# Optimization experiments

Measured on AMD Instinct MI355X. Metric: run time of the kernel, lower is better.

The kernel has to match this reference:

```python
import jax, jax.numpy as jnp
import numpy as np

BAND_WIDTH = 0.05
EPS = 1e-5
NORM_EPS = 1e-12  # F.normalize clamp_min


def _l2_normalize_channels(x):
    # x: (B, C, D, H, W); normalize over channel dim=1 like F.normalize(p=2, dim=1)
    n = jnp.sqrt(jnp.sum(x * x, axis=1, keepdims=True))
    return x / jnp.maximum(n, NORM_EPS)


def setup_inputs() -> dict:
    key = jax.random.key(0)
    k1, k2, k3 = jax.random.split(key, 3)
    B, C, D, H, W = 2, 256, 8, 8, 8
    P, K = 128, 512  # n_patches iterations, k=512 sampled voxels per patch
    S = D * H * W  # 512 spatial voxels
    t2_feat = jax.random.normal(k1, (B, C, D, H, W), dtype=jnp.float32)
    t1_feat = jax.random.normal(k2, (B, C, D, H, W), dtype=jnp.float32)
    idx = jax.random.randint(k3, (P, K), 0, S, dtype=jnp.int32)
    return {"t2_feat": t2_feat, "t1_feat": t1_feat, "idx": idx}


def reference(t2_feat, t1_feat, idx):
    B, C = t2_feat.shape[:2]
    # normalize channels, flatten spatial dims: (B, C, S)
    t2 = _l2_normalize_channels(t2_feat).reshape(B, C, -1)
    t1 = _l2_normalize_channels(t1_feat).reshape(B, C, -1)
    # gather the same random voxels for both modalities: (B, C, P, K)
    t2p = t2[:, :, idx]
    t1p = t1[:, :, idx]
    # batched cosine similarity: bmm(t2p^T, t1p) per patch -> (P, B, K, K)
    cs = jnp.einsum('bcpk,bcpl->pbkl', t2p, t1p)
    e = jnp.exp(cs / BAND_WIDTH)
    pos = jnp.diagonal(e, axis1=2, axis2=3)  # (P, B, K) exp of positives
    # InfoNCE over columns (torch dim=1 of (B,K,K)) and rows (dim=2)
    info_nce1 = pos / jnp.sum(e, axis=2)
    info_nce2 = pos / jnp.sum(e, axis=3)
    info_nce = 0.5 * (info_nce1 + info_nce2)
    # per-patch mean of -log, then mean over patches == global mean
    return jnp.mean(-jnp.log(info_nce + EPS))
```

## Files before the change

kernel.cpp:

```cpp
#include <hip/hip_runtime.h>

typedef __attribute__((ext_vector_type(8))) short bf16x8;
typedef __attribute__((ext_vector_type(4))) float f32x4;
typedef __attribute__((ext_vector_type(4))) ushort u16x4;

#define C_DIM 256
#define S_DIM 512
#define P_DIM 128
#define K_DIM 512
#define INV_BW 20.0f
#define EPS_LOSS 1e-5f

#define OFF_DIAG   0
#define OFF_EBF    1024
#define OFF_ETBF   263168
#define OFF_PART   525312
#define OFF_BAR    525376

__device__ inline ushort f2bf(float f) {
  union { float f; uint u; } v; v.f = f;
  return (ushort)((v.u + 0x7FFF + ((v.u >> 16) & 1)) >> 16);
}
__device__ inline float bf2f(ushort u) {
  union { uint u; float f; } v; v.u = ((uint)u) << 16;
  return v.f;
}

__global__ __launch_bounds__(256) void gram_exp_kernel(
    const float* __restrict__ t2, const float* __restrict__ t1,
    ushort* __restrict__ Ebf, ushort* __restrict__ ETbf,
    float* __restrict__ diag, int* __restrict__ bar) {
  __shared__ ushort A_[32][264];
  __shared__ ushort B_[32][264];
  __shared__ float sA[32], sB[32];
  int blk = blockIdx.x, tid = threadIdx.x;
  if (blk == 0 && tid == 0) bar[0] = 0;
  int mb = blk & 15, nb = (blk >> 4) & 15, b = blk >> 8;
  int m0 = mb * 32, c0 = nb * 32;
  {
    const float* pa = t2 + (b * C_DIM + tid) * S_DIM + m0;
    const float* pb = t1 + (b * C_DIM + tid) * S_DIM + c0;
    #pragma unroll
    for (int q = 0; q < 8; ++q) {
      float4 va = *reinterpret_cast<const float4*>(pa + q * 4);
      float4 vb = *reinterpret_cast<const float4*>(pb + q * 4);
      A_[q * 4 + 0][tid] = f2bf(va.x); A_[q * 4 + 1][tid] = f2bf(va.y);
      A_[q * 4 + 2][tid] = f2bf(va.z); A_[q * 4 + 3][tid] = f2bf(va.w);
      B_[q * 4 + 0][tid] = f2bf(vb.x); B_[q * 4 + 1][tid] = f2bf(vb.y);
      B_[q * 4 + 2][tid] = f2bf(vb.z); B_[q * 4 + 3][tid] = f2bf(vb.w);
    }
  }
  __syncthreads();
  if (tid < 64) {
    const ushort* row = (tid < 32) ? &A_[tid][0] : &B_[tid - 32][0];
    float a0 = 0.f, a1 = 0.f, a2 = 0.f, a3 = 0.f;
    #pragma unroll
    for (int k = 0; k < 64; ++k) {
      u16x4 v = *reinterpret_cast<const u16x4*>(row + k * 4);
      float x0 = bf2f(v.x), x1 = bf2f(v.y), x2 = bf2f(v.z), x3 = bf2f(v.w);
      a0 += x0 * x0; a1 += x1 * x1; a2 += x2 * x2; a3 += x3 * x3;
    }
    float sc = 1.0f / fmaxf(sqrtf((a0 + a1) + (a2 + a3)), 1e-12f);
    if (tid < 32) sA[tid] = sc; else sB[tid - 32] = sc;
  }
  __syncthreads();
  int wave = tid >> 6, lane = tid & 63;
  int tm = wave & 1, tn = wave >> 1;
  int lr = lane & 15, lo = lane >> 4;
  f32x4 acc = {0.f, 0.f, 0.f, 0.f};
  #pragma unroll
  for (int k = 0; k < 8; ++k) {
    bf16x8 af = *reinterpret_cast<const bf16x8*>(&A_[tm * 16 + lr][lo * 8 + k * 32]);
    bf16x8 bv = *reinterpret_cast<const bf16x8*>(&B_[tn * 16 + lr][lo * 8 + k * 32]);
    acc = __builtin_amdgcn_mfma_f32_16x16x32_bf16(af, bv, acc, 0, 0, 0);
  }
  int mg0 = m0 + tm * 16, cg0 = c0 + tn * 16;
  float bs = sB[tn * 16 + lr];
  ushort* Eb  = Ebf  + b * (S_DIM * S_DIM);
  ushort* ETb = ETbf + b * (S_DIM * S_DIM);
  float e[4]; ushort eb[4];
  #pragma unroll
  for (int r = 0; r < 4; ++r) {
    int rl = tm * 16 + lo * 4 + r;
    float ev = __expf(acc[r] * sA[rl] * bs * INV_BW);
    e[r] = ev; eb[r] = f2bf(ev);
    Eb[(m0 + rl) * S_DIM + cg0 + lr] = eb[r];
  }
  u16x4 pk = {eb[0], eb[1], eb[2], eb[3]};
  *reinterpret_cast<u16x4*>(&ETb[(cg0 + lr) * S_DIM + mg0 + lo * 4]) = pk;
  if (mg0 == cg0 && (lr >> 2) == lo) diag[b * S_DIM + mg0 + lr] = e[lr & 3];
}

__global__ __launch_bounds__(1024) void denom_loss_kernel(
    const ushort* __restrict__ Ebf, const ushort* __restrict__ ETbf,
    const int* __restrict__ idx, const float* __restrict__ diag,
    float* __restrict__ part, int* __restrict__ bar, float* __restrict__ out) {
  __shared__ int hist[16][516];
  __shared__ ushort cb[16][520];
  __shared__ float D1L[16][132], D2L[16][132];
  int blk = blockIdx.x, tid = threadIdx.x;
  int m = blk & 7, b = (blk >> 3) & 1, q = blk >> 4;
  int p0 = m * 16;
  int wave = tid >> 6, lane = tid & 63;
  int lr = lane & 15, lo = lane >> 4;
  {
    int p = tid >> 6, l = tid & 63;
    int* hp = &hist[p][0];
    #pragma unroll
    for (int j = 0; j < 8; ++j) hp[l * 8 + j] = 0;
    __syncthreads();
    const int* ip = idx + (p0 + p) * K_DIM + l;
    #pragma unroll
    for (int j = 0; j < 8; ++j) atomicAdd(&hp[ip[j * 64]], 1);
    __syncthreads();
    #pragma unroll
    for (int j = 0; j < 8; ++j) {
      int col = l * 8 + j;
      cb[p][col] = f2bf((float)hp[col]);
    }
  }
  __syncthreads();
  {
    int z = wave >> 3, jt = wave & 7;
    int col0g = q * 128 + jt * 16, col0l = jt * 16;
    const ushort* Bmat = (z ? Ebf : ETbf) + b * (S_DIM * S_DIM);
    const ushort* bptr = Bmat + (col0g + lr) * S_DIM + lo * 8;
    f32x4 acc = {0.f, 0.f, 0.f, 0.f};
    #pragma unroll
    for (int k = 0; k < 16; ++k) {
      bf16x8 af = *reinterpret_cast<const bf16x8*>(&cb[lr][lo * 8 + k * 32]);
      bf16x8 bv = *reinterpret_cast<const bf16x8*>(bptr + k * 32);
      acc = __builtin_amdgcn_mfma_f32_16x16x32_bf16(af, bv, acc, 0, 0, 0);
    }
    #pragma unroll
    for (int r = 0; r < 4; ++r) {
      int p = lo * 4 + r;
      if (z) D2L[p][col0l + lr] = acc[r];
      else   D1L[p][col0l + lr] = acc[r];
    }
  }
  __syncthreads();
  {
    int p = tid >> 6, l = tid & 63;
    const int* ip = idx + (p0 + p) * K_DIM + l;
    float acc = 0.f;
    #pragma unroll
    for (int j = 0; j < 8; ++j) {
      int s = ip[j * 64];
      if ((s >> 7) == q) {
        int sl = s & 127;
        float pos = diag[b * S_DIM + s];
        float d1 = D1L[p][sl];
        float d2 = D2L[p][sl];
        acc += __logf(0.5f * (pos / d1 + pos / d2) + EPS_LOSS);
      }
    }
    for (int o = 32; o; o >>= 1) acc += __shfl_down(acc, o);
    __shared__ float red[16];
    __shared__ int lastflag;
    if (lane == 0) red[wave] = acc;
    __syncthreads();
    if (tid == 0) {
      float tsum = 0.f;
      #pragma unroll
      for (int i = 0; i < 16; ++i) tsum += red[i];
      atomicExch(&part[blk], tsum);
      __threadfence();
      int old = atomicAdd(&bar[0], 1);
      lastflag = (old == 63);
    }
    __syncthreads();
    if (lastflag && tid < 64) {
      __threadfence();
      float v = atomicAdd(&part[tid], 0.0f);
      for (int o = 32; o; o >>= 1) v += __shfl_down(v, o);
      if (tid == 0) out[0] = -v * (1.0f / (P_DIM * 2.0f * K_DIM));
    }
  }
}

extern "C" void kernel_launch(void* const* d_in, const int* in_sizes, int n_in,
                              void* d_out, int out_size, void* d_ws, size_t ws_size,
                              hipStream_t stream) {
  const float* t2 = (const float*)d_in[0];
  const float* t1 = (const float*)d_in[1];
  const int* idx  = (const int*)d_in[2];
  float* ws = (float*)d_ws;
  float*  diag   = ws + OFF_DIAG;
  ushort* Ebf    = (ushort*)(ws + OFF_EBF);
  ushort* ETbf   = (ushort*)(ws + OFF_ETBF);
  float*  part   = ws + OFF_PART;
  int*    bar    = (int*)(ws + OFF_BAR);

  gram_exp_kernel<<<512, 256, 0, stream>>>(t2, t1, Ebf, ETbf, diag, bar);
  denom_loss_kernel<<<64, 1024, 0, stream>>>(Ebf, ETbf, idx, diag, part, bar,
                                             (float*)d_out);
}
```

Before: 29.13 us.

## Enlarge gram tile to 64x32 with A-fragment reuse; split denom kernel finer

```diff
diff --git a/kernel.cpp b/kernel.cpp
--- a/kernel.cpp
+++ b/kernel.cpp
@@ -15,7 +15,7 @@
 #define OFF_EBF    1024
 #define OFF_ETBF   263168
 #define OFF_PART   525312
-#define OFF_BAR    525376
+#define OFF_BAR    525440
 
 __device__ inline ushort f2bf(float f) {
   union { float f; uint u; } v; v.f = f;
@@ -30,29 +30,32 @@
     const float* __restrict__ t2, const float* __restrict__ t1,
     ushort* __restrict__ Ebf, ushort* __restrict__ ETbf,
     float* __restrict__ diag, int* __restrict__ bar) {
-  __shared__ ushort A_[32][264];
-  __shared__ ushort B_[32][264];
-  __shared__ float sA[32], sB[32];
+  __shared__ ushort A_[64][260];
+  __shared__ ushort B_[32][260];
+  __shared__ float sA[64], sB[32];
   int blk = blockIdx.x, tid = threadIdx.x;
   if (blk == 0 && tid == 0) bar[0] = 0;
-  int mb = blk & 15, nb = (blk >> 4) & 15, b = blk >> 8;
-  int m0 = mb * 32, c0 = nb * 32;
+  int mb = blk & 7, nb = (blk >> 3) & 15, b = blk >> 7;
+  int m0 = mb * 64, c0 = nb * 32;
   {
     const float* pa = t2 + (b * C_DIM + tid) * S_DIM + m0;
     const float* pb = t1 + (b * C_DIM + tid) * S_DIM + c0;
     #pragma unroll
-    for (int q = 0; q < 8; ++q) {
+    for (int q = 0; q < 16; ++q) {
       float4 va = *reinterpret_cast<const float4*>(pa + q * 4);
-      float4 vb = *reinterpret_cast<const float4*>(pb + q * 4);
       A_[q * 4 + 0][tid] = f2bf(va.x); A_[q * 4 + 1][tid] = f2bf(va.y);
       A_[q * 4 + 2][tid] = f2bf(va.z); A_[q * 4 + 3][tid] = f2bf(va.w);
+    }
+    #pragma unroll
+    for (int q = 0; q < 8; ++q) {
+      float4 vb = *reinterpret_cast<const float4*>(pb + q * 4);
       B_[q * 4 + 0][tid] = f2bf(vb.x); B_[q * 4 + 1][tid] = f2bf(vb.y);
       B_[q * 4 + 2][tid] = f2bf(vb.z); B_[q * 4 + 3][tid] = f2bf(vb.w);
     }
   }
   __syncthreads();
-  if (tid < 64) {
-    const ushort* row = (tid < 32) ? &A_[tid][0] : &B_[tid - 32][0];
+  if (tid < 96) {
+    const ushort* row = (tid < 64) ? &A_[tid][0] : &B_[tid - 64][0];
     float a0 = 0.f, a1 = 0.f, a2 = 0.f, a3 = 0.f;
     #pragma unroll
     for (int k = 0; k < 64; ++k) {
@@ -61,68 +64,74 @@
       a0 += x0 * x0; a1 += x1 * x1; a2 += x2 * x2; a3 += x3 * x3;
     }
     float sc = 1.0f / fmaxf(sqrtf((a0 + a1) + (a2 + a3)), 1e-12f);
-    if (tid < 32) sA[tid] = sc; else sB[tid - 32] = sc;
+    if (tid < 64) sA[tid] = sc; else sB[tid - 64] = sc;
   }
   __syncthreads();
   int wave = tid >> 6, lane = tid & 63;
-  int tm = wave & 1, tn = wave >> 1;
   int lr = lane & 15, lo = lane >> 4;
-  f32x4 acc = {0.f, 0.f, 0.f, 0.f};
+  bf16x8 afr[8];
   #pragma unroll
-  for (int k = 0; k < 8; ++k) {
-    bf16x8 af = *reinterpret_cast<const bf16x8*>(&A_[tm * 16 + lr][lo * 8 + k * 32]);
-    bf16x8 bv = *reinterpret_cast<const bf16x8*>(&B_[tn * 16 + lr][lo * 8 + k * 32]);
-    acc = __builtin_amdgcn_mfma_f32_16x16x32_bf16(af, bv, acc, 0, 0, 0);
-  }
-  int mg0 = m0 + tm * 16, cg0 = c0 + tn * 16;
-  float bs = sB[tn * 16 + lr];
+  for (int k = 0; k < 8; ++k)
+    afr[k] = *reinterpret_cast<const bf16x8*>(&A_[wave * 16 + lr][lo * 8 + k * 32]);
   ushort* Eb  = Ebf  + b * (S_DIM * S_DIM);
   ushort* ETb = ETbf + b * (S_DIM * S_DIM);
-  float e[4]; ushort eb[4];
+  int mg0 = m0 + wave * 16;
   #pragma unroll
-  for (int r = 0; r < 4; ++r) {
-    int rl = tm * 16 + lo * 4 + r;
-    float ev = __expf(acc[r] * sA[rl] * bs * INV_BW);
-    e[r] = ev; eb[r] = f2bf(ev);
-    Eb[(m0 + rl) * S_DIM + cg0 + lr] = eb[r];
-  }
-  u16x4 pk = {eb[0], eb[1], eb[2], eb[3]};
-  *reinterpret_cast<u16x4*>(&ETb[(cg0 + lr) * S_DIM + mg0 + lo * 4]) = pk;
-  if (mg0 == cg0 && (lr >> 2) == lo) diag[b * S_DIM + mg0 + lr] = e[lr & 3];
-}
-
-__global__ __launch_bounds__(1024) void denom_loss_kernel(
+  for (int tn = 0; tn < 2; ++tn) {
+    f32x4 acc = {0.f, 0.f, 0.f, 0.f};
+    #pragma unroll
+    for (int k = 0; k < 8; ++k) {
+      bf16x8 bv = *reinterpret_cast<const bf16x8*>(&B_[tn * 16 + lr][lo * 8 + k * 32]);
+      acc = __builtin_amdgcn_mfma_f32_16x16x32_bf16(afr[k], bv, acc, 0, 0, 0);
+    }
+    int cg0 = c0 + tn * 16;
+    float bs = sB[tn * 16 + lr];
+    float e[4]; ushort eb[4];
+    #pragma unroll
+    for (int r = 0; r < 4; ++r) {
+      int rl = wave * 16 + lo * 4 + r;
+      float ev = __expf(acc[r] * sA[rl] * bs * INV_BW);
+      e[r] = ev; eb[r] = f2bf(ev);
+      Eb[(m0 + rl) * S_DIM + cg0 + lr] = eb[r];
+    }
+    u16x4 pk = {eb[0], eb[1], eb[2], eb[3]};
+    *reinterpret_cast<u16x4*>(&ETb[(cg0 + lr) * S_DIM + mg0 + lo * 4]) = pk;
+    if (mg0 == cg0 && (lr >> 2) == lo) diag[b * S_DIM + mg0 + lr] = e[lr & 3];
+  }
+}
+
+__global__ __launch_bounds__(512) void denom_loss_kernel(
     const ushort* __restrict__ Ebf, const ushort* __restrict__ ETbf,
     const int* __restrict__ idx, const float* __restrict__ diag,
     float* __restrict__ part, int* __restrict__ bar, float* __restrict__ out) {
   __shared__ int hist[16][516];
   __shared__ ushort cb[16][520];
-  __shared__ float D1L[16][132], D2L[16][132];
+  __shared__ float D1L[16][68], D2L[16][68];
   int blk = blockIdx.x, tid = threadIdx.x;
-  int m = blk & 7, b = (blk >> 3) & 1, q = blk >> 4;
+  int m = blk & 7, b = (blk >> 3) & 1, o = blk >> 4;
   int p0 = m * 16;
   int wave = tid >> 6, lane = tid & 63;
   int lr = lane & 15, lo = lane >> 4;
   {
-    int p = tid >> 6, l = tid & 63;
+    int p = tid >> 5, l = tid & 31;
     int* hp = &hist[p][0];
     #pragma unroll
-    for (int j = 0; j < 8; ++j) hp[l * 8 + j] = 0;
+    for (int j = 0; j < 16; ++j) hp[l * 16 + j] = 0;
     __syncthreads();
     const int* ip = idx + (p0 + p) * K_DIM + l;
     #pragma unroll
-    for (int j = 0; j < 8; ++j) atomicAdd(&hp[ip[j * 64]], 1);
-    __syncthreads();
-    #pragma unroll
-    for (int j = 0; j < 8; ++j) {
-      int col = l * 8 + j;
+    for (int j = 0; j < 16; ++j) atomicAdd(&hp[ip[j * 32]], 1);
+    __syncthreads();
+    #pragma unroll
+    for (int j = 0; j < 16; ++j) {
+      int col = l * 16 + j;
       cb[p][col] = f2bf((float)hp[col]);
     }
   }
   __syncthreads();
   {
-    int z = wave >> 3, jt = wave & 7;
-    int col0g = q * 128 + jt * 16, col0l = jt * 16;
+    int z = wave >> 2, jt = wave & 3;
+    int col0g = o * 64 + jt * 16, col0l = jt * 16;
     const ushort* Bmat = (z ? Ebf : ETbf) + b * (S_DIM * S_DIM);
     const ushort* bptr = Bmat + (col0g + lr) * S_DIM + lo * 8;
     f32x4 acc = {0.f, 0.f, 0.f, 0.f};
@@ -141,40 +150,46 @@
   }
   __syncthreads();
   {
-    int p = tid >> 6, l = tid & 63;
+    int p = tid >> 5, l = tid & 31;
     const int* ip = idx + (p0 + p) * K_DIM + l;
     float acc = 0.f;
     #pragma unroll
-    for (int j = 0; j < 8; ++j) {
-      int s = ip[j * 64];
-      if ((s >> 7) == q) {
-        int sl = s & 127;
+    for (int j = 0; j < 16; ++j) {
+      int s = ip[j * 32];
+      if ((s >> 6) == o) {
+        int sl = s & 63;
         float pos = diag[b * S_DIM + s];
         float d1 = D1L[p][sl];
         float d2 = D2L[p][sl];
         acc += __logf(0.5f * (pos / d1 + pos / d2) + EPS_LOSS);
       }
     }
-    for (int o = 32; o; o >>= 1) acc += __shfl_down(acc, o);
-    __shared__ float red[16];
+    for (int off = 32; off; off >>= 1) acc += __shfl_down(acc, off);
+    __shared__ float red[8];
     __shared__ int lastflag;
     if (lane == 0) red[wave] = acc;
     __syncthreads();
     if (tid == 0) {
       float tsum = 0.f;
       #pragma unroll
-      for (int i = 0; i < 16; ++i) tsum += red[i];
+      for (int i = 0; i < 8; ++i) tsum += red[i];
       atomicExch(&part[blk], tsum);
       __threadfence();
       int old = atomicAdd(&bar[0], 1);
-      lastflag = (old == 63);
-    }
-    __syncthreads();
-    if (lastflag && tid < 64) {
+      lastflag = (old == 127);
+    }
+    __syncthreads();
+    if (lastflag) {
       __threadfence();
-      float v = atomicAdd(&part[tid], 0.0f);
-      for (int o = 32; o; o >>= 1) v += __shfl_down(v, o);
-      if (tid == 0) out[0] = -v * (1.0f / (P_DIM * 2.0f * K_DIM));
+      float v = (tid < P_DIM) ? atomicAdd(&part[tid], 0.0f) : 0.0f;
+      for (int off = 32; off; off >>= 1) v += __shfl_down(v, off);
+      __shared__ float red2[8];
+      if (lane == 0) red2[wave] = v;
+      __syncthreads();
+      if (tid == 0) {
+        float tsum = red2[0] + red2[1];
+        out[0] = -tsum * (1.0f / (P_DIM * 2.0f * K_DIM));
+      }
     }
   }
 }
@@ -192,7 +207,7 @@
   float*  part   = ws + OFF_PART;
   int*    bar    = (int*)(ws + OFF_BAR);
 
-  gram_exp_kernel<<<512, 256, 0, stream>>>(t2, t1, Ebf, ETbf, diag, bar);
-  denom_loss_kernel<<<64, 1024, 0, stream>>>(Ebf, ETbf, idx, diag, part, bar,
+  gram_exp_kernel<<<256, 256, 0, stream>>>(t2, t1, Ebf, ETbf, diag, bar);
+  denom_loss_kernel<<<128, 512, 0, stream>>>(Ebf, ETbf, idx, diag, part, bar,
                                              (float*)d_out);
 }
```

Result: slower. 30.36 us (+4.2%).
